# Kernel optimization log

Hardware: AMD Instinct MI355X
Metric: run time of the kernel (lower is better)

## Reference

```python
import jax, jax.numpy as jnp
import numpy as np

EMBED = 1024
HEADS = 16
HEAD_DIM = EMBED // HEADS
LN_EPS = 1e-5


def _layer_norm(x, g, b):
    m = jnp.mean(x, axis=-1, keepdims=True)
    v = jnp.mean((x - m) ** 2, axis=-1, keepdims=True)
    return (x - m) / jnp.sqrt(v + LN_EPS) * g + b


def _rope(x):
    # x: (b, H, n, D); standard rotary: freqs repeated (cat(freqs, freqs)), rotate_half
    D = x.shape[-1]
    n = x.shape[2]
    inv_freq = 1.0 / (10000.0 ** (jnp.arange(0, D, 2, dtype=jnp.float32) / D))
    freqs = jnp.arange(n, dtype=jnp.float32)[:, None] * inv_freq[None, :]  # (n, D/2)
    emb = jnp.concatenate([freqs, freqs], axis=-1)  # (n, D)
    cos, sin = jnp.cos(emb), jnp.sin(emb)
    rot = jnp.concatenate([-x[..., D // 2:], x[..., : D // 2]], axis=-1)
    return x * cos + rot * sin


def setup_inputs() -> dict:
    key = jax.random.key(0)
    ks = jax.random.split(key, 8)
    E = EMBED
    s_in = 1.0 / np.sqrt(E)
    return {
        "x": jax.random.normal(ks[0], (2, 2048, E), dtype=jnp.float32),
        "in_proj_w": jax.random.uniform(ks[1], (3 * E, E), jnp.float32, -s_in, s_in),
        "in_proj_b": jnp.zeros((3 * E,), jnp.float32),
        "out_proj_w": jax.random.uniform(ks[2], (E, E), jnp.float32, -s_in, s_in),
        "out_proj_b": jnp.zeros((E,), jnp.float32),
        "geglu_w": jax.random.uniform(ks[3], (2 * E, E), jnp.float32, -s_in, s_in),
        "geglu_b": jnp.zeros((2 * E,), jnp.float32),
        "ln1_g": jnp.ones((E,), jnp.float32),
        "ln1_b": jnp.zeros((E,), jnp.float32),
        "ln2_g": jnp.ones((E,), jnp.float32),
        "ln2_b": jnp.zeros((E,), jnp.float32),
    }


def reference(x, in_proj_w, in_proj_b, out_proj_w, out_proj_b,
              geglu_w, geglu_b, ln1_g, ln1_b, ln2_g, ln2_b):
    b, n, E = x.shape
    H, D = HEADS, HEAD_DIM

    # RoPE applied to raw x (q = k = v = x in the module)
    xh = x.reshape(b, n, H, D).transpose(0, 2, 1, 3)  # (b,H,n,D)
    qr = _rope(xh)
    kr = qr  # q and k are identical pre-projection
    q = qr.transpose(0, 2, 1, 3).reshape(b, n, E)
    k = kr.transpose(0, 2, 1, 3).reshape(b, n, E)
    v = x

    # MultiheadAttention (batch-first semantics): in-proj, per-head SDPA, out-proj
    w_q, w_k, w_v = jnp.split(in_proj_w, 3, axis=0)
    b_q, b_k, b_v = jnp.split(in_proj_b, 3, axis=0)
    qp = (q @ w_q.T + b_q).reshape(b, n, H, D).transpose(0, 2, 1, 3)
    kp = (k @ w_k.T + b_k).reshape(b, n, H, D).transpose(0, 2, 1, 3)
    vp = (v @ w_v.T + b_v).reshape(b, n, H, D).transpose(0, 2, 1, 3)
    scores = jnp.einsum("bhqd,bhkd->bhqk", qp, kp) / jnp.sqrt(jnp.float32(D))
    attn = jax.nn.softmax(scores, axis=-1)
    ctx = jnp.einsum("bhqk,bhkd->bhqd", attn, vp)
    ctx = ctx.transpose(0, 2, 1, 3).reshape(b, n, E)
    attn_out = ctx @ out_proj_w.T + out_proj_b

    # residual + LN1
    h = _layer_norm(x + attn_out, ln1_g, ln1_b)

    # GeGLU: Linear(E -> 2E), chunk, value * gelu(gate) (exact erf gelu like torch)
    proj = h @ geglu_w.T + geglu_b
    val, gate = jnp.split(proj, 2, axis=-1)
    fc_out = val * jax.nn.gelu(gate, approximate=False)

    # residual + LN2
    return _layer_norm(h + fc_out, ln2_g, ln2_b)
```

## Files before the change

kernel.cpp:

```cpp
#include <hip/hip_runtime.h>


typedef __bf16 bf16;
typedef bf16 bf16x8 __attribute__((ext_vector_type(8)));
typedef bf16 bf16x4 __attribute__((ext_vector_type(4)));
typedef float f32x4 __attribute__((ext_vector_type(4)));
typedef float f32x16 __attribute__((ext_vector_type(16)));

#define EMB 1024
#define SEQ 2048
#define NTOK 4096
#define NH 16
#define HD 64

__device__ __forceinline__ f32x4 mfma16(bf16x8 a, bf16x8 b, f32x4 c) {
  return __builtin_amdgcn_mfma_f32_16x16x32_bf16(a, b, c, 0, 0, 0);
}
__device__ __forceinline__ f32x16 mfma32(bf16x8 a, bf16x8 b, f32x16 c) {
  return __builtin_amdgcn_mfma_f32_32x32x16_bf16(a, b, c, 0, 0, 0);
}

__device__ __forceinline__ void gll16(const void* g, void* l) {
  __builtin_amdgcn_global_load_lds(
      (const __attribute__((address_space(1))) void*)g,
      (__attribute__((address_space(3))) void*)l, 16, 0, 0);
}

__device__ __forceinline__ unsigned pk2(float a, float b) {
  union { bf16 h[2]; unsigned u; } t;
  t.h[0] = (bf16)a; t.h[1] = (bf16)b;
  return t.u;
}


__global__ __launch_bounds__(256) void rope_cast(
    const float* __restrict__ x, bf16* __restrict__ xb, bf16* __restrict__ qr) {
  int idx = blockIdx.x * 256 + threadIdx.x;
  int row = idx >> 9;
  int i = idx & 511;
  int h = i >> 5, d2 = i & 31;
  int pos = row & (SEQ - 1);
  int c0 = h * HD + d2;
  size_t base = (size_t)row * EMB;
  float x0 = x[base + c0], x1 = x[base + c0 + 32];
  float invf = exp2f(-(float)d2 * 0.4152410118609203f);
  float ang = (float)pos * invf;
  float sn, cs;
  sincosf(ang, &sn, &cs);
  qr[base + c0] = (bf16)(x0 * cs - x1 * sn);
  qr[base + c0 + 32] = (bf16)(x1 * cs + x0 * sn);
  xb[base + c0] = (bf16)x0;
  xb[base + c0 + 32] = (bf16)x1;
}

__global__ __launch_bounds__(256) void cast_all(
    const float* __restrict__ w0, const float* __restrict__ w1,
    const float* __restrict__ w2, bf16* __restrict__ o0,
    bf16* __restrict__ o1, bf16* __restrict__ o2) {
  int i = (blockIdx.x * 256 + threadIdx.x) * 4;
  const float* s; bf16* d; int off;
  if (i < 3 * 1024 * 1024) { s = w0; d = o0; off = i; }
  else if (i < 4 * 1024 * 1024) { s = w1; d = o1; off = i - 3 * 1024 * 1024; }
  else { s = w2; d = o2; off = i - 4 * 1024 * 1024; }
  float4 f = *(const float4*)(s + off);
  d[off] = (bf16)f.x; d[off + 1] = (bf16)f.y;
  d[off + 2] = (bf16)f.z; d[off + 3] = (bf16)f.w;
}

__global__ __launch_bounds__(256) void gemm_in(
    const bf16* __restrict__ Aq, const bf16* __restrict__ Ax,
    const bf16* __restrict__ W, const float* __restrict__ bias,
    bf16* __restrict__ qb, bf16* __restrict__ kv) {
  __shared__ bf16 As[128 * 32];
  __shared__ bf16 Bs[128 * 32];
  const int tid = threadIdx.x, lane = tid & 63, wave = tid >> 6;
  const int quad = lane >> 4, l16 = lane & 15;
  const int m0 = blockIdx.y * 128, n0 = blockIdx.x * 128;
  const bf16* A = (n0 < 2048) ? Aq : Ax;
  const int K = 1024;
  const int wm = (wave >> 1) * 64, wn = (wave & 1) * 64;
  const int srow = wave * 32 + (lane >> 2);
  const int scol = (lane & 3) * 8;
  f32x4 acc[4][4] = {};
  for (int k0 = 0; k0 < K; k0 += 32) {
    __syncthreads();
    gll16(A + (size_t)(m0 + srow) * K + k0 + scol, As + wave * 1024);
    gll16(A + (size_t)(m0 + srow + 16) * K + k0 + scol, As + wave * 1024 + 512);
    gll16(W + (size_t)(n0 + srow) * K + k0 + scol, Bs + wave * 1024);
    gll16(W + (size_t)(n0 + srow + 16) * K + k0 + scol, Bs + wave * 1024 + 512);
    __syncthreads();
    bf16x8 af[4], bw[4];
#pragma unroll
    for (int t = 0; t < 4; ++t) {
      af[t] = *(const bf16x8*)(As + (wm + t * 16 + l16) * 32 + quad * 8);
      bw[t] = *(const bf16x8*)(Bs + (wn + t * 16 + l16) * 32 + quad * 8);
    }
#pragma unroll
    for (int mt = 0; mt < 4; ++mt)
#pragma unroll
      for (int nt = 0; nt < 4; ++nt)
        acc[mt][nt] = mfma16(af[mt], bw[nt], acc[mt][nt]);
  }
  if (n0 < 1024) {
#pragma unroll
    for (int mt = 0; mt < 4; ++mt)
      for (int nt = 0; nt < 4; ++nt) {
        const int n = n0 + wn + nt * 16 + l16;
        const float bv = bias[n];
#pragma unroll
        for (int r = 0; r < 4; ++r) {
          const int m = m0 + wm + mt * 16 + quad * 4 + r;
          qb[(size_t)m * 1024 + n] = (bf16)((acc[mt][nt][r] + bv) * 0.125f);
        }
      }
  } else if (n0 < 2048) {
#pragma unroll
    for (int mt = 0; mt < 4; ++mt)
      for (int nt = 0; nt < 4; ++nt) {
        const int n = n0 + wn + nt * 16 + l16;
        const float bv = bias[n];
        const int kd = n - 1024, hh = kd >> 6, d = kd & 63;
        const int dc = d >> 3, dl = d & 7;
#pragma unroll
        for (int r = 0; r < 4; ++r) {
          const int m = m0 + wm + mt * 16 + quad * 4 + r;
          const int bb = m >> 11, s = m & 2047;
          const int t = s >> 6, kr = s & 63;
          const size_t base = ((size_t)((bb * 16 + hh) * 32 + t)) * 8192;
          kv[base + kr * 64 + ((dc ^ (kr & 7)) << 3) + dl] =
              (bf16)((acc[mt][nt][r] + bv) * 1.4426950408889634f);
        }
      }
  } else {
#pragma unroll
    for (int mt = 0; mt < 4; ++mt)
      for (int nt = 0; nt < 4; ++nt) {
        const int n = n0 + wn + nt * 16 + l16;
        const float bv = bias[n];
        const int vd = n - 2048, hh = vd >> 6, d = vd & 63;
        const int m = m0 + wm + mt * 16 + quad * 4;
        const int bb = m >> 11, s = m & 2047;
        const int t = s >> 6, kt = s & 63;
        const int g = kt >> 4, w = kt & 15;
        const int c = 2 * g + ((w >> 2) & 1);
        const int slot = (w & 8) ? 4 : 0;
        const size_t base = ((size_t)((bb * 16 + hh) * 32 + t)) * 8192 + 4096;
        bf16x4 pkv;
#pragma unroll
        for (int r = 0; r < 4; ++r) pkv[r] = (bf16)(acc[mt][nt][r] + bv);
        *(bf16x4*)(kv + base + d * 64 + ((c ^ (d & 7)) << 3) + slot) = pkv;
      }
  }
}

__global__ __launch_bounds__(256) void gemm_bt(
    const bf16* __restrict__ A, const bf16* __restrict__ W,
    const float* __restrict__ bias,
    float* __restrict__ outF, bf16* __restrict__ outB,
    int M, int N, int K) {
  __shared__ bf16 As[128 * 32];
  __shared__ bf16 Bs[128 * 32];
  const int tid = threadIdx.x, lane = tid & 63, wave = tid >> 6;
  const int quad = lane >> 4, l16 = lane & 15;
  const int m0 = blockIdx.y * 128, n0 = blockIdx.x * 128;
  const int wm = (wave >> 1) * 64, wn = (wave & 1) * 64;
  const int srow = wave * 32 + (lane >> 2);
  const int scol = (lane & 3) * 8;
  f32x4 acc[4][4] = {};
  for (int k0 = 0; k0 < K; k0 += 32) {
    __syncthreads();
    gll16(A + (size_t)(m0 + srow) * K + k0 + scol, As + wave * 1024);
    gll16(A + (size_t)(m0 + srow + 16) * K + k0 + scol, As + wave * 1024 + 512);
    gll16(W + (size_t)(n0 + srow) * K + k0 + scol, Bs + wave * 1024);
    gll16(W + (size_t)(n0 + srow + 16) * K + k0 + scol, Bs + wave * 1024 + 512);
    __syncthreads();
    bf16x8 af[4], bw[4];
#pragma unroll
    for (int t = 0; t < 4; ++t) {
      af[t] = *(const bf16x8*)(As + (wm + t * 16 + l16) * 32 + quad * 8);
      bw[t] = *(const bf16x8*)(Bs + (wn + t * 16 + l16) * 32 + quad * 8);
    }
#pragma unroll
    for (int mt = 0; mt < 4; ++mt)
#pragma unroll
      for (int nt = 0; nt < 4; ++nt)
        acc[mt][nt] = mfma16(af[mt], bw[nt], acc[mt][nt]);
  }
#pragma unroll
  for (int mt = 0; mt < 4; ++mt)
    for (int nt = 0; nt < 4; ++nt) {
      const int n = n0 + wn + nt * 16 + l16;
      const float bv = bias ? bias[n] : 0.0f;
#pragma unroll
      for (int r = 0; r < 4; ++r) {
        const int m = m0 + wm + mt * 16 + quad * 4 + r;
        const float v = acc[mt][nt][r] + bv;
        if (outF) outF[(size_t)m * N + n] = v;
        if (outB) outB[(size_t)m * N + n] = (bf16)v;
      }
    }
}

__global__ __launch_bounds__(256) void gemm_bt64(
    const bf16* __restrict__ A, const bf16* __restrict__ W,
    const float* __restrict__ bias, float* __restrict__ outF,
    int M, int N, int K) {
  __shared__ bf16 As[128 * 32];
  __shared__ bf16 Bs[64 * 32];
  const int tid = threadIdx.x, lane = tid & 63, wave = tid >> 6;
  const int quad = lane >> 4, l16 = lane & 15;
  const int m0 = blockIdx.y * 128, n0 = blockIdx.x * 64;
  const int wm = (wave >> 1) * 64, wn = (wave & 1) * 32;
  const int srow = wave * 32 + (lane >> 2);
  const int srowB = wave * 16 + (lane >> 2);
  const int scol = (lane & 3) * 8;
  f32x4 acc[4][2] = {};
  for (int k0 = 0; k0 < K; k0 += 32) {
    __syncthreads();
    gll16(A + (size_t)(m0 + srow) * K + k0 + scol, As + wave * 1024);
    gll16(A + (size_t)(m0 + srow + 16) * K + k0 + scol, As + wave * 1024 + 512);
    gll16(W + (size_t)(n0 + srowB) * K + k0 + scol, Bs + wave * 512);
    __syncthreads();
    bf16x8 af[4], bw[2];
#pragma unroll
    for (int t = 0; t < 4; ++t)
      af[t] = *(const bf16x8*)(As + (wm + t * 16 + l16) * 32 + quad * 8);
#pragma unroll
    for (int t = 0; t < 2; ++t)
      bw[t] = *(const bf16x8*)(Bs + (wn + t * 16 + l16) * 32 + quad * 8);
#pragma unroll
    for (int mt = 0; mt < 4; ++mt)
#pragma unroll
      for (int nt = 0; nt < 2; ++nt)
        acc[mt][nt] = mfma16(af[mt], bw[nt], acc[mt][nt]);
  }
#pragma unroll
  for (int mt = 0; mt < 4; ++mt)
    for (int nt = 0; nt < 2; ++nt) {
      const int n = n0 + wn + nt * 16 + l16;
      const float bv = bias[n];
#pragma unroll
      for (int r = 0; r < 4; ++r) {
        const int m = m0 + wm + mt * 16 + quad * 4 + r;
        outF[(size_t)m * N + n] = acc[mt][nt][r] + bv;
      }
    }
}

__global__ __launch_bounds__(256, 3) void attn13(
    const bf16* __restrict__ Q, const bf16* __restrict__ KV,
    bf16* __restrict__ ctx) {
  __shared__ __align__(16) bf16 kvb[3][8192];
  __shared__ float Linv[4][32];
  const int tid = threadIdx.x, lane = tid & 63, wave = tid >> 6;
  const int hi = lane >> 5, l31 = lane & 31, l7 = lane & 7;
  const int bid = blockIdx.x;
  const int hb = (bid & 7) * 4 + ((bid >> 3) & 3);
  const int qt = bid >> 5;
  const int h = hb & 15, b = hb >> 4;

  bf16x8 qf[4];
  {
    const int qrow = qt * 128 + wave * 32 + l31;
    const bf16* qp = Q + (size_t)(b * SEQ + qrow) * 1024 + h * HD + hi * 8;
#pragma unroll
    for (int t = 0; t < 4; ++t) qf[t] = *(const bf16x8*)(qp + t * 16);
  }
  asm volatile("s_waitcnt vmcnt(0)" ::: "memory");

  const int soff = tid * 8;
  const bf16* kvg = KV + ((size_t)(b * NH + h) * 32) * 8192 + soff;
#pragma unroll
  for (int i = 0; i < 4; ++i)
    gll16(kvg + i * 2048, kvb[0] + soff + i * 2048);
#pragma unroll
  for (int i = 0; i < 4; ++i)
    gll16(kvg + 8192 + i * 2048, kvb[1] + soff + i * 2048);

  f32x16 o0 = {}, o1 = {};
  float lpart = 0.0f;
  const f32x16 zf = {};
  int rd = 0, wr = 2;

  for (int t = 0; t < 32; ++t) {
    if (t < 31) asm volatile("s_waitcnt vmcnt(4)" ::: "memory");
    else        asm volatile("s_waitcnt vmcnt(0)" ::: "memory");
    __builtin_amdgcn_s_barrier();
    __builtin_amdgcn_sched_barrier(0);
    if (t + 2 < 32) {
      const bf16* src = kvg + (size_t)(t + 2) * 8192;
      bf16* dst = kvb[wr] + soff;
#pragma unroll
      for (int i = 0; i < 4; ++i) gll16(src + i * 2048, dst + i * 2048);
    }
    const bf16* ks = kvb[rd];
    const bf16* vs = ks + 4096;
    f32x16 s0, s1;
    __builtin_amdgcn_s_setprio(1);
    {
      const int swc = (hi ^ l7) * 8;
      bf16x8 k0 = *(const bf16x8*)(ks + l31 * 64 + swc);
      bf16x8 k1 = *(const bf16x8*)(ks + (32 + l31) * 64 + swc);
      s0 = mfma32(k0, qf[0], zf);
      s1 = mfma32(k1, qf[0], zf);
    }
#pragma unroll
    for (int tt = 1; tt < 4; ++tt) {
      const int swc = ((tt * 2 + hi) ^ l7) * 8;
      bf16x8 k0 = *(const bf16x8*)(ks + l31 * 64 + swc);
      bf16x8 k1 = *(const bf16x8*)(ks + (32 + l31) * 64 + swc);
      s0 = mfma32(k0, qf[tt], s0);
      s1 = mfma32(k1, qf[tt], s1);
    }
    __builtin_amdgcn_s_setprio(0);
    unsigned u[16];
#pragma unroll
    for (int g = 0; g < 8; ++g) {
      const int base = (g & 3) * 4;
      float e0, e1, e2, e3;
      if (g < 4) {
        e0 = __builtin_amdgcn_exp2f(s0[base]);
        e1 = __builtin_amdgcn_exp2f(s0[base + 1]);
        e2 = __builtin_amdgcn_exp2f(s0[base + 2]);
        e3 = __builtin_amdgcn_exp2f(s0[base + 3]);
      } else {
        e0 = __builtin_amdgcn_exp2f(s1[base]);
        e1 = __builtin_amdgcn_exp2f(s1[base + 1]);
        e2 = __builtin_amdgcn_exp2f(s1[base + 2]);
        e3 = __builtin_amdgcn_exp2f(s1[base + 3]);
      }
      lpart += (e0 + e1) + (e2 + e3);
      u[g * 2] = pk2(e0, e1);
      u[g * 2 + 1] = pk2(e2, e3);
    }
    __builtin_amdgcn_s_setprio(1);
#pragma unroll
    for (int kk = 0; kk < 4; ++kk) {
      union { unsigned w[4]; bf16x8 v; } fw;
      fw.w[0] = u[4 * kk]; fw.w[1] = u[4 * kk + 1];
      fw.w[2] = u[4 * kk + 2]; fw.w[3] = u[4 * kk + 3];
      const int c16 = (2 * kk + hi) ^ l7;
      bf16x8 v0 = *(const bf16x8*)(vs + l31 * 64 + c16 * 8);
      bf16x8 v1 = *(const bf16x8*)(vs + (32 + l31) * 64 + c16 * 8);
      o0 = mfma32(fw.v, v0, o0);
      o1 = mfma32(fw.v, v1, o1);
    }
    __builtin_amdgcn_s_setprio(0);
    rd = (rd + 1 == 3) ? 0 : rd + 1;
    wr = (wr + 1 == 3) ? 0 : wr + 1;
  }
  float ltot = lpart + __shfl_xor(lpart, 32, 64);
  if (lane < 32) Linv[wave][lane] = 1.0f / ltot;
#pragma unroll
  for (int r = 0; r < 16; ++r) {
    const int qloc = (r & 3) + 8 * (r >> 2) + 4 * hi;
    const float inv = Linv[wave][qloc];
    const int qrow = qt * 128 + wave * 32 + qloc;
    bf16* cp = ctx + (size_t)(b * SEQ + qrow) * EMB + h * HD;
    cp[l31] = (bf16)(o0[r] * inv);
    cp[32 + l31] = (bf16)(o1[r] * inv);
  }
}

__global__ __launch_bounds__(256) void ln1_k(
    const float* __restrict__ x, const float* __restrict__ ao,
    const float* __restrict__ g, const float* __restrict__ bta,
    float* __restrict__ hF, bf16* __restrict__ hB) {
  int row = blockIdx.x, tid = threadIdx.x;
  const float* xr = x + (size_t)row * EMB;
  const float* ar = ao + (size_t)row * EMB;
  float v[4], s = 0.0f, s2 = 0.0f;
#pragma unroll
  for (int i = 0; i < 4; ++i) {
    float t = xr[tid + i * 256] + ar[tid + i * 256];
    v[i] = t; s += t; s2 += t * t;
  }
#pragma unroll
  for (int off = 1; off < 64; off <<= 1) {
    s += __shfl_xor(s, off, 64);
    s2 += __shfl_xor(s2, off, 64);
  }
  __shared__ float red[8];
  int wave = tid >> 6, lane = tid & 63;
  if (lane == 0) { red[wave] = s; red[4 + wave] = s2; }
  __syncthreads();
  s = red[0] + red[1] + red[2] + red[3];
  s2 = red[4] + red[5] + red[6] + red[7];
  float mean = s * (1.0f / EMB);
  float var = s2 * (1.0f / EMB) - mean * mean;
  float inv = rsqrtf(var + 1e-5f);
#pragma unroll
  for (int i = 0; i < 4; ++i) {
    int c = tid + i * 256;
    float t = (v[i] - mean) * inv * g[c] + bta[c];
    hF[(size_t)row * EMB + c] = t;
    hB[(size_t)row * EMB + c] = (bf16)t;
  }
}

__global__ __launch_bounds__(256) void geglu_ln2(
    const float* __restrict__ h, const bf16* __restrict__ proj,
    const float* __restrict__ g, const float* __restrict__ bta,
    float* __restrict__ out) {
  int row = blockIdx.x, tid = threadIdx.x;
  const float* hr = h + (size_t)row * EMB;
  const bf16* pr = proj + (size_t)row * 2048;
  float v[4], s = 0.0f, s2 = 0.0f;
#pragma unroll
  for (int i = 0; i < 4; ++i) {
    int c = tid + i * 256;
    float val = (float)pr[c];
    float gate = (float)pr[1024 + c];
    float ge = 0.5f * gate * (1.0f + erff(gate * 0.70710678f));
    float t = hr[c] + val * ge;
    v[i] = t; s += t; s2 += t * t;
  }
#pragma unroll
  for (int off = 1; off < 64; off <<= 1) {
    s += __shfl_xor(s, off, 64);
    s2 += __shfl_xor(s2, off, 64);
  }
  __shared__ float red[8];
  int wave = tid >> 6, lane = tid & 63;
  if (lane == 0) { red[wave] = s; red[4 + wave] = s2; }
  __syncthreads();
  s = red[0] + red[1] + red[2] + red[3];
  s2 = red[4] + red[5] + red[6] + red[7];
  float mean = s * (1.0f / EMB);
  float var = s2 * (1.0f / EMB) - mean * mean;
  float inv = rsqrtf(var + 1e-5f);
#pragma unroll
  for (int i = 0; i < 4; ++i) {
    int c = tid + i * 256;
    out[(size_t)row * EMB + c] = (v[i] - mean) * inv * g[c] + bta[c];
  }
}

extern "C" void kernel_launch(void* const* d_in, const int* in_sizes, int n_in,
                              void* d_out, int out_size, void* d_ws, size_t ws_size,
                              hipStream_t stream) {
  const float* x = (const float*)d_in[0];
  const float* inW = (const float*)d_in[1];
  const float* inB = (const float*)d_in[2];
  const float* outW = (const float*)d_in[3];
  const float* opB = (const float*)d_in[4];
  const float* ggW = (const float*)d_in[5];
  const float* ggB = (const float*)d_in[6];
  const float* g1 = (const float*)d_in[7];
  const float* b1 = (const float*)d_in[8];
  const float* g2 = (const float*)d_in[9];
  const float* b2 = (const float*)d_in[10];
  float* out = (float*)d_out;
  char* ws = (char*)d_ws;
  const size_t MB = 1ull << 20;
  bf16* xb = (bf16*)(ws);
  bf16* hB = (bf16*)(ws);
  bf16* qr = (bf16*)(ws + 8 * MB);
  bf16* ctx = (bf16*)(ws + 8 * MB);
  bf16* wI = (bf16*)(ws + 16 * MB);
  bf16* wO = (bf16*)(ws + 22 * MB);
  bf16* wG = (bf16*)(ws + 24 * MB);
  bf16* qb = (bf16*)(ws + 28 * MB);
  bf16* kv = (bf16*)(ws + 36 * MB);
  bf16* projB = (bf16*)(ws + 28 * MB);
  float* ao = (float*)(ws + 52 * MB);

  rope_cast<<<NTOK * 512 / 256, 256, 0, stream>>>(x, xb, qr);
  cast_all<<<6144, 256, 0, stream>>>(inW, outW, ggW, wI, wO, wG);
  gemm_in<<<dim3(24, 32), 256, 0, stream>>>(qr, xb, wI, inB, qb, kv);
  attn13<<<512, 256, 0, stream>>>(qb, kv, ctx);
  gemm_bt64<<<dim3(16, 32), 256, 0, stream>>>(ctx, wO, opB, ao,
                                              NTOK, 1024, 1024);
  ln1_k<<<NTOK, 256, 0, stream>>>(x, ao, g1, b1, ao, hB);
  gemm_bt<<<dim3(16, 32), 256, 0, stream>>>(hB, wG, ggB, nullptr, projB,
                                            NTOK, 2048, 1024);
  geglu_ln2<<<NTOK, 256, 0, stream>>>(ao, projB, g2, b2, out);
}
```

Before: 276.3 us.

## Fuse prep kernels, double-buffer larger attention KV tiles, reuse gemm_bt for out-proj

Merges the RoPE/cast kernel and the weight-cast kernel into one launch to cut a kernel launch and let the two overlap. The attention kernel moves from a 3-stage ring of 64-key tiles to 2-stage double buffering of 128-key tiles, with a second barrier before each refill and occupancy hint lowered to 2 blocks. The output projection now uses the 128x128 gemm_bt tile instead of the dedicated 128x64 kernel, halving block count. The larger LDS footprint and fewer blocks for out-proj may reduce latency hiding.

```diff
diff --git a/kernel.cpp b/kernel.cpp
--- a/kernel.cpp
+++ b/kernel.cpp
@@ -32,39 +32,39 @@
   return t.u;
 }
 
-
-__global__ __launch_bounds__(256) void rope_cast(
-    const float* __restrict__ x, bf16* __restrict__ xb, bf16* __restrict__ qr) {
-  int idx = blockIdx.x * 256 + threadIdx.x;
-  int row = idx >> 9;
-  int i = idx & 511;
-  int h = i >> 5, d2 = i & 31;
-  int pos = row & (SEQ - 1);
-  int c0 = h * HD + d2;
-  size_t base = (size_t)row * EMB;
-  float x0 = x[base + c0], x1 = x[base + c0 + 32];
-  float invf = exp2f(-(float)d2 * 0.4152410118609203f);
-  float ang = (float)pos * invf;
-  float sn, cs;
-  sincosf(ang, &sn, &cs);
-  qr[base + c0] = (bf16)(x0 * cs - x1 * sn);
-  qr[base + c0 + 32] = (bf16)(x1 * cs + x0 * sn);
-  xb[base + c0] = (bf16)x0;
-  xb[base + c0 + 32] = (bf16)x1;
-}
-
-__global__ __launch_bounds__(256) void cast_all(
+__global__ __launch_bounds__(256) void prep_all(
+    const float* __restrict__ x, bf16* __restrict__ xb, bf16* __restrict__ qr,
     const float* __restrict__ w0, const float* __restrict__ w1,
     const float* __restrict__ w2, bf16* __restrict__ o0,
     bf16* __restrict__ o1, bf16* __restrict__ o2) {
-  int i = (blockIdx.x * 256 + threadIdx.x) * 4;
-  const float* s; bf16* d; int off;
-  if (i < 3 * 1024 * 1024) { s = w0; d = o0; off = i; }
-  else if (i < 4 * 1024 * 1024) { s = w1; d = o1; off = i - 3 * 1024 * 1024; }
-  else { s = w2; d = o2; off = i - 4 * 1024 * 1024; }
-  float4 f = *(const float4*)(s + off);
-  d[off] = (bf16)f.x; d[off + 1] = (bf16)f.y;
-  d[off + 2] = (bf16)f.z; d[off + 3] = (bf16)f.w;
+  const int bid = blockIdx.x;
+  if (bid < 8192) {
+    int idx = bid * 256 + threadIdx.x;
+    int row = idx >> 9;
+    int i = idx & 511;
+    int h = i >> 5, d2 = i & 31;
+    int pos = row & (SEQ - 1);
+    int c0 = h * HD + d2;
+    size_t base = (size_t)row * EMB;
+    float x0 = x[base + c0], x1 = x[base + c0 + 32];
+    float invf = exp2f(-(float)d2 * 0.4152410118609203f);
+    float ang = (float)pos * invf;
+    float sn, cs;
+    sincosf(ang, &sn, &cs);
+    qr[base + c0] = (bf16)(x0 * cs - x1 * sn);
+    qr[base + c0 + 32] = (bf16)(x1 * cs + x0 * sn);
+    xb[base + c0] = (bf16)x0;
+    xb[base + c0 + 32] = (bf16)x1;
+  } else {
+    int i = ((bid - 8192) * 256 + threadIdx.x) * 4;
+    const float* s; bf16* d; int off;
+    if (i < 3 * 1024 * 1024) { s = w0; d = o0; off = i; }
+    else if (i < 4 * 1024 * 1024) { s = w1; d = o1; off = i - 3 * 1024 * 1024; }
+    else { s = w2; d = o2; off = i - 4 * 1024 * 1024; }
+    float4 f = *(const float4*)(s + off);
+    d[off] = (bf16)f.x; d[off + 1] = (bf16)f.y;
+    d[off + 2] = (bf16)f.z; d[off + 3] = (bf16)f.w;
+  }
 }
 
 __global__ __launch_bounds__(256) void gemm_in(
@@ -201,56 +201,10 @@
     }
 }
 
-__global__ __launch_bounds__(256) void gemm_bt64(
-    const bf16* __restrict__ A, const bf16* __restrict__ W,
-    const float* __restrict__ bias, float* __restrict__ outF,
-    int M, int N, int K) {
-  __shared__ bf16 As[128 * 32];
-  __shared__ bf16 Bs[64 * 32];
-  const int tid = threadIdx.x, lane = tid & 63, wave = tid >> 6;
-  const int quad = lane >> 4, l16 = lane & 15;
-  const int m0 = blockIdx.y * 128, n0 = blockIdx.x * 64;
-  const int wm = (wave >> 1) * 64, wn = (wave & 1) * 32;
-  const int srow = wave * 32 + (lane >> 2);
-  const int srowB = wave * 16 + (lane >> 2);
-  const int scol = (lane & 3) * 8;
-  f32x4 acc[4][2] = {};
-  for (int k0 = 0; k0 < K; k0 += 32) {
-    __syncthreads();
-    gll16(A + (size_t)(m0 + srow) * K + k0 + scol, As + wave * 1024);
-    gll16(A + (size_t)(m0 + srow + 16) * K + k0 + scol, As + wave * 1024 + 512);
-    gll16(W + (size_t)(n0 + srowB) * K + k0 + scol, Bs + wave * 512);
-    __syncthreads();
-    bf16x8 af[4], bw[2];
-#pragma unroll
-    for (int t = 0; t < 4; ++t)
-      af[t] = *(const bf16x8*)(As + (wm + t * 16 + l16) * 32 + quad * 8);
-#pragma unroll
-    for (int t = 0; t < 2; ++t)
-      bw[t] = *(const bf16x8*)(Bs + (wn + t * 16 + l16) * 32 + quad * 8);
-#pragma unroll
-    for (int mt = 0; mt < 4; ++mt)
-#pragma unroll
-      for (int nt = 0; nt < 2; ++nt)
-        acc[mt][nt] = mfma16(af[mt], bw[nt], acc[mt][nt]);
-  }
-#pragma unroll
-  for (int mt = 0; mt < 4; ++mt)
-    for (int nt = 0; nt < 2; ++nt) {
-      const int n = n0 + wn + nt * 16 + l16;
-      const float bv = bias[n];
-#pragma unroll
-      for (int r = 0; r < 4; ++r) {
-        const int m = m0 + wm + mt * 16 + quad * 4 + r;
-        outF[(size_t)m * N + n] = acc[mt][nt][r] + bv;
-      }
-    }
-}
-
-__global__ __launch_bounds__(256, 3) void attn13(
+__global__ __launch_bounds__(256, 2) void attn14(
     const bf16* __restrict__ Q, const bf16* __restrict__ KV,
     bf16* __restrict__ ctx) {
-  __shared__ __align__(16) bf16 kvb[3][8192];
+  __shared__ __align__(16) bf16 kvb[2][16384];
   __shared__ float Linv[4][32];
   const int tid = threadIdx.x, lane = tid & 63, wave = tid >> 6;
   const int hi = lane >> 5, l31 = lane & 31, l7 = lane & 7;
@@ -271,83 +225,87 @@
   const int soff = tid * 8;
   const bf16* kvg = KV + ((size_t)(b * NH + h) * 32) * 8192 + soff;
 #pragma unroll
-  for (int i = 0; i < 4; ++i)
+  for (int i = 0; i < 8; ++i)
     gll16(kvg + i * 2048, kvb[0] + soff + i * 2048);
 #pragma unroll
-  for (int i = 0; i < 4; ++i)
-    gll16(kvg + 8192 + i * 2048, kvb[1] + soff + i * 2048);
+  for (int i = 0; i < 8; ++i)
+    gll16(kvg + 16384 + i * 2048, kvb[1] + soff + i * 2048);
 
   f32x16 o0 = {}, o1 = {};
   float lpart = 0.0f;
   const f32x16 zf = {};
-  int rd = 0, wr = 2;
-
-  for (int t = 0; t < 32; ++t) {
-    if (t < 31) asm volatile("s_waitcnt vmcnt(4)" ::: "memory");
+
+  for (int t = 0; t < 16; ++t) {
+    if (t < 15) asm volatile("s_waitcnt vmcnt(8)" ::: "memory");
     else        asm volatile("s_waitcnt vmcnt(0)" ::: "memory");
     __builtin_amdgcn_s_barrier();
     __builtin_amdgcn_sched_barrier(0);
-    if (t + 2 < 32) {
-      const bf16* src = kvg + (size_t)(t + 2) * 8192;
-      bf16* dst = kvb[wr] + soff;
-#pragma unroll
-      for (int i = 0; i < 4; ++i) gll16(src + i * 2048, dst + i * 2048);
+    const bf16* tb = kvb[t & 1];
+#pragma unroll
+    for (int half = 0; half < 2; ++half) {
+      const bf16* ks = tb + half * 8192;
+      const bf16* vs = ks + 4096;
+      f32x16 s0, s1;
+      __builtin_amdgcn_s_setprio(1);
+      {
+        const int swc = (hi ^ l7) * 8;
+        bf16x8 k0 = *(const bf16x8*)(ks + l31 * 64 + swc);
+        bf16x8 k1 = *(const bf16x8*)(ks + (32 + l31) * 64 + swc);
+        s0 = mfma32(k0, qf[0], zf);
+        s1 = mfma32(k1, qf[0], zf);
+      }
+#pragma unroll
+      for (int tt = 1; tt < 4; ++tt) {
+        const int swc = ((tt * 2 + hi) ^ l7) * 8;
+        bf16x8 k0 = *(const bf16x8*)(ks + l31 * 64 + swc);
+        bf16x8 k1 = *(const bf16x8*)(ks + (32 + l31) * 64 + swc);
+        s0 = mfma32(k0, qf[tt], s0);
+        s1 = mfma32(k1, qf[tt], s1);
+      }
+      __builtin_amdgcn_s_setprio(0);
+      unsigned u[16];
+#pragma unroll
+      for (int g = 0; g < 8; ++g) {
+        const int base = (g & 3) * 4;
+        float e0, e1, e2, e3;
+        if (g < 4) {
+          e0 = __builtin_amdgcn_exp2f(s0[base]);
+          e1 = __builtin_amdgcn_exp2f(s0[base + 1]);
+          e2 = __builtin_amdgcn_exp2f(s0[base + 2]);
+          e3 = __builtin_amdgcn_exp2f(s0[base + 3]);
+        } else {
+          e0 = __builtin_amdgcn_exp2f(s1[base]);
+          e1 = __builtin_amdgcn_exp2f(s1[base + 1]);
+          e2 = __builtin_amdgcn_exp2f(s1[base + 2]);
+          e3 = __builtin_amdgcn_exp2f(s1[base + 3]);
+        }
+        lpart += (e0 + e1) + (e2 + e3);
+        u[g * 2] = pk2(e0, e1);
+        u[g * 2 + 1] = pk2(e2, e3);
+      }
+      __builtin_amdgcn_s_setprio(1);
+#pragma unroll
+      for (int kk = 0; kk < 4; ++kk) {
+        union { unsigned w[4]; bf16x8 v; } fw;
+        fw.w[0] = u[4 * kk]; fw.w[1] = u[4 * kk + 1];
+        fw.w[2] = u[4 * kk + 2]; fw.w[3] = u[4 * kk + 3];
+        const int c16 = (2 * kk + hi) ^ l7;
+        bf16x8 v0 = *(const bf16x8*)(vs + l31 * 64 + c16 * 8);
+        bf16x8 v1 = *(const bf16x8*)(vs + (32 + l31) * 64 + c16 * 8);
+        o0 = mfma32(fw.v, v0, o0);
+        o1 = mfma32(fw.v, v1, o1);
+      }
+      __builtin_amdgcn_s_setprio(0);
     }
-    const bf16* ks = kvb[rd];
-    const bf16* vs = ks + 4096;
-    f32x16 s0, s1;
-    __builtin_amdgcn_s_setprio(1);
-    {
-      const int swc = (hi ^ l7) * 8;
-      bf16x8 k0 = *(const bf16x8*)(ks + l31 * 64 + swc);
-      bf16x8 k1 = *(const bf16x8*)(ks + (32 + l31) * 64 + swc);
-      s0 = mfma32(k0, qf[0], zf);
-      s1 = mfma32(k1, qf[0], zf);
+    __builtin_amdgcn_sched_barrier(0);
+    __builtin_amdgcn_s_barrier();
+    __builtin_amdgcn_sched_barrier(0);
+    if (t + 2 < 16) {
+      const bf16* src = kvg + (size_t)(t + 2) * 16384;
+      bf16* dst = kvb[t & 1] + soff;
+#pragma unroll
+      for (int i = 0; i < 8; ++i) gll16(src + i * 2048, dst + i * 2048);
     }
-#pragma unroll
-    for (int tt = 1; tt < 4; ++tt) {
-      const int swc = ((tt * 2 + hi) ^ l7) * 8;
-      bf16x8 k0 = *(const bf16x8*)(ks + l31 * 64 + swc);
-      bf16x8 k1 = *(const bf16x8*)(ks + (32 + l31) * 64 + swc);
-      s0 = mfma32(k0, qf[tt], s0);
-      s1 = mfma32(k1, qf[tt], s1);
-    }
-    __builtin_amdgcn_s_setprio(0);
-    unsigned u[16];
-#pragma unroll
-    for (int g = 0; g < 8; ++g) {
-      const int base = (g & 3) * 4;
-      float e0, e1, e2, e3;
-      if (g < 4) {
-        e0 = __builtin_amdgcn_exp2f(s0[base]);
-        e1 = __builtin_amdgcn_exp2f(s0[base + 1]);
-        e2 = __builtin_amdgcn_exp2f(s0[base + 2]);
-        e3 = __builtin_amdgcn_exp2f(s0[base + 3]);
-      } else {
-        e0 = __builtin_amdgcn_exp2f(s1[base]);
-        e1 = __builtin_amdgcn_exp2f(s1[base + 1]);
-        e2 = __builtin_amdgcn_exp2f(s1[base + 2]);
-        e3 = __builtin_amdgcn_exp2f(s1[base + 3]);
-      }
-      lpart += (e0 + e1) + (e2 + e3);
-      u[g * 2] = pk2(e0, e1);
-      u[g * 2 + 1] = pk2(e2, e3);
-    }
-    __builtin_amdgcn_s_setprio(1);
-#pragma unroll
-    for (int kk = 0; kk < 4; ++kk) {
-      union { unsigned w[4]; bf16x8 v; } fw;
-      fw.w[0] = u[4 * kk]; fw.w[1] = u[4 * kk + 1];
-      fw.w[2] = u[4 * kk + 2]; fw.w[3] = u[4 * kk + 3];
-      const int c16 = (2 * kk + hi) ^ l7;
-      bf16x8 v0 = *(const bf16x8*)(vs + l31 * 64 + c16 * 8);
-      bf16x8 v1 = *(const bf16x8*)(vs + (32 + l31) * 64 + c16 * 8);
-      o0 = mfma32(fw.v, v0, o0);
-      o1 = mfma32(fw.v, v1, o1);
-    }
-    __builtin_amdgcn_s_setprio(0);
-    rd = (rd + 1 == 3) ? 0 : rd + 1;
-    wr = (wr + 1 == 3) ? 0 : wr + 1;
   }
   float ltot = lpart + __shfl_xor(lpart, 32, 64);
   if (lane < 32) Linv[wave][lane] = 1.0f / ltot;
@@ -465,12 +423,12 @@
   bf16* projB = (bf16*)(ws + 28 * MB);
   float* ao = (float*)(ws + 52 * MB);
 
-  rope_cast<<<NTOK * 512 / 256, 256, 0, stream>>>(x, xb, qr);
-  cast_all<<<6144, 256, 0, stream>>>(inW, outW, ggW, wI, wO, wG);
+  prep_all<<<8192 + 6144, 256, 0, stream>>>(x, xb, qr, inW, outW, ggW,
+                                            wI, wO, wG);
   gemm_in<<<dim3(24, 32), 256, 0, stream>>>(qr, xb, wI, inB, qb, kv);
-  attn13<<<512, 256, 0, stream>>>(qb, kv, ctx);
-  gemm_bt64<<<dim3(16, 32), 256, 0, stream>>>(ctx, wO, opB, ao,
-                                              NTOK, 1024, 1024);
+  attn14<<<512, 256, 0, stream>>>(qb, kv, ctx);
+  gemm_bt<<<dim3(8, 32), 256, 0, stream>>>(ctx, wO, opB, ao, nullptr,
+                                           NTOK, 1024, 1024);
   ln1_k<<<NTOK, 256, 0, stream>>>(x, ao, g1, b1, ao, hB);
   gemm_bt<<<dim3(16, 32), 256, 0, stream>>>(hB, wG, ggB, nullptr, projB,
                                             NTOK, 2048, 1024);
```

Result: no change. 274.3 us (-0.7%).
